# Kernel optimization log

Measured on AMD Instinct MI355X. Metric: run time of the kernel, lower is better.

## Reference

```python
import jax, jax.numpy as jnp
import numpy as np

N = 100_000      # nodes
E = 1_600_000    # edges (avg degree 16)
H = 128          # hidden_dim
L = 2            # num_layers
G = 64           # graphs in batch
BN_EPS = 1e-5


def setup_inputs() -> dict:
    key = jax.random.key(0)
    ks = jax.random.split(key, 20)
    x = jax.random.normal(ks[0], (N, 1), jnp.float32)
    edge_index = jax.random.randint(ks[1], (2, E), 0, N, dtype=jnp.int64)
    edge_attr = jax.random.uniform(ks[2], (E, 1), jnp.float32)
    batch = jnp.sort(jax.random.randint(ks[3], (N,), 0, G, dtype=jnp.int64))
    s = 1.0 / np.sqrt(H)
    return {
        "x": x, "edge_index": edge_index, "edge_attr": edge_attr, "batch": batch,
        "enc_w": jax.random.normal(ks[4], (1, H), jnp.float32),
        "enc_b": jnp.zeros((H,), jnp.float32),
        "eenc_w": jax.random.normal(ks[5], (1, H), jnp.float32),
        "eenc_b": jnp.zeros((H,), jnp.float32),
        "eps": jnp.zeros((L,), jnp.float32),  # train_eps=True, init 0
        "w1": jax.random.normal(ks[6], (L, H, H), jnp.float32) * s,
        "b1": jnp.zeros((L, H), jnp.float32),
        "w2": jax.random.normal(ks[7], (L, H, H), jnp.float32) * s,
        "b2": jnp.zeros((L, H), jnp.float32),
        "gamma": jnp.ones((L, H), jnp.float32),
        "beta": jnp.zeros((L, H), jnp.float32),
        "cw1": jax.random.normal(ks[8], (H, H // 2), jnp.float32) * s,
        "cb1": jnp.zeros((H // 2,), jnp.float32),
        "cw2": jax.random.normal(ks[9], (H // 2, 1), jnp.float32) * (1.0 / np.sqrt(H // 2)),
        "cb2": jnp.zeros((1,), jnp.float32),
    }


def reference(x, edge_index, edge_attr, batch,
              enc_w, enc_b, eenc_w, eenc_b,
              eps, w1, b1, w2, b2, gamma, beta,
              cw1, cb1, cw2, cb2):
    # Inference mode: dropout = identity, BatchNorm uses running stats (mean=0, var=1).
    h = x @ enc_w + enc_b                 # [N, H] node encoder
    ea = edge_attr @ eenc_w + eenc_b      # [E, H] edge encoder
    src, dst = edge_index[0], edge_index[1]
    inv_std = 1.0 / jnp.sqrt(1.0 + BN_EPS)
    for l in range(L):
        # GINEConv: out = MLP((1+eps)*x + sum_j relu(x_j + e_ij))
        msg = jax.nn.relu(h[src] + ea)                         # [E, H] gather + fuse
        agg = jax.ops.segment_sum(msg, dst, num_segments=N)    # [N, H] scatter-sum
        z = (1.0 + eps[l]) * h + agg
        z = jax.nn.relu(z @ w1[l] + b1[l]) @ w2[l] + b2[l]      # GIN MLP
        h = jax.nn.relu(gamma[l] * z * inv_std + beta[l])       # BN (eval) + ReLU
    # global mean pool over graphs
    cnt = jax.ops.segment_sum(jnp.ones((N, 1), h.dtype), batch, num_segments=G)
    pooled = jax.ops.segment_sum(h, batch, num_segments=G) / jnp.maximum(cnt, 1.0)
    hc = jax.nn.relu(pooled @ cw1 + cb1)
    out = jax.nn.sigmoid(hc @ cw2 + cb2)
    return out.squeeze(-1)                # [G]
```

## Files before the change

### kernel.cpp

```cpp
#include <hip/hip_runtime.h>

#define HDIM 128
#define NGRAPH 64
#define INVSTD 0.99999500003749972f
#define WTPAD 136
#define WSLOT (128 * WTPAD)
#define BKN 512
#define EPB 4096

typedef unsigned short ushort_t;
typedef unsigned int uint_t;
typedef unsigned char uchar_t;
typedef __attribute__((ext_vector_type(8))) short bf16x8;
typedef __attribute__((ext_vector_type(4))) float f32x4;
typedef __attribute__((ext_vector_type(2))) float f32x2;

__device__ __forceinline__ float bf2f(uint_t u) {
    return __int_as_float((int)(u << 16));
}
__device__ __forceinline__ float bf2f_hi(uint_t u) {
    return __int_as_float((int)(u & 0xFFFF0000u));
}
__device__ __forceinline__ uint_t f2bf(float f) {
    uint_t x = __float_as_uint(f);
    return (x + 0x7FFFu + ((x >> 16) & 1u)) >> 16;
}
__device__ __forceinline__ uint_t pack2(float a, float b) {
    return f2bf(a) | (f2bf(b) << 16);
}
__device__ __forceinline__ uint_t pack4fp8(float a, float b, float c, float d) {
    int v = __builtin_amdgcn_cvt_pk_fp8_f32(a, b, 0, false);
    v = __builtin_amdgcn_cvt_pk_fp8_f32(c, d, v, true);
    return (uint_t)v;
}

__global__ void k_encode(const float* __restrict__ x, const float* __restrict__ ew,
                         const float* __restrict__ enb, const float* __restrict__ ebe,
                         ushort_t* __restrict__ hb, uchar_t* __restrict__ hq, int N) {
    int tid = blockIdx.x * blockDim.x + threadIdx.x;
    int stride = gridDim.x * blockDim.x;
    int q = tid & 15;
    float4 wa = ((const float4*)ew)[2 * q];
    float4 wb = ((const float4*)ew)[2 * q + 1];
    float4 ba = ((const float4*)enb)[2 * q];
    float4 bb = ((const float4*)enb)[2 * q + 1];
    float4 ea = ((const float4*)ebe)[2 * q];
    float4 eb2 = ((const float4*)ebe)[2 * q + 1];
    ba.x += ea.x; ba.y += ea.y; ba.z += ea.z; ba.w += ea.w;
    bb.x += eb2.x; bb.y += eb2.y; bb.z += eb2.z; bb.w += eb2.w;
    int total = N * 16;
    for (int t = tid; t < total; t += stride) {
        int n = t >> 4;
        float xv = x[n];
        float v0 = fmaf(xv, wa.x, ba.x), v1 = fmaf(xv, wa.y, ba.y);
        float v2 = fmaf(xv, wa.z, ba.z), v3 = fmaf(xv, wa.w, ba.w);
        float v4 = fmaf(xv, wb.x, bb.x), v5 = fmaf(xv, wb.y, bb.y);
        float v6 = fmaf(xv, wb.z, bb.z), v7 = fmaf(xv, wb.w, bb.w);
        uint4 o;
        o.x = pack2(v0, v1); o.y = pack2(v2, v3);
        o.z = pack2(v4, v5); o.w = pack2(v6, v7);
        ((uint4*)(hb + (size_t)n * HDIM))[q] = o;
        uint2 o8;
        o8.x = pack4fp8(v0, v1, v2, v3);
        o8.y = pack4fp8(v4, v5, v6, v7);
        ((uint2*)(hq + (size_t)n * HDIM))[q] = o8;
    }
}

__global__ void k_prepw(const float* __restrict__ w1, const float* __restrict__ w2,
                        ushort_t* __restrict__ wtg) {
    int t = blockIdx.x * 256 + threadIdx.x;
    if (t >= 4 * 16384) return;
    int w = t >> 14, idx = t & 16383;
    int k = idx >> 7, n = idx & 127;
    const float* src = ((w & 1) ? w2 : w1) + (size_t)(w >> 1) * 16384;
    wtg[(size_t)w * WSLOT + n * WTPAD + k] = (ushort_t)f2bf(src[idx]);
}

__global__ __launch_bounds__(256) void k_cnt(const int* __restrict__ ei, int* __restrict__ btot,
                                             int nb, int E) {
    __shared__ int hist[256];
    hist[threadIdx.x] = 0;
    __syncthreads();
    int e0 = blockIdx.x * EPB;
    for (int i = threadIdx.x; i < EPB; i += 256) {
        int e = e0 + i;
        if (e < E) atomicAdd(&hist[ei[E + e] / BKN], 1);
    }
    __syncthreads();
    int c = hist[threadIdx.x];
    if (threadIdx.x < nb && c > 0) atomicAdd(&btot[threadIdx.x], c);
}

__global__ void k_bscan(const int* __restrict__ btot, int* __restrict__ segs, int nb, int E) {
    __shared__ int sm[256];
    int t = threadIdx.x;
    int v = (t < nb) ? btot[t] : 0;
    sm[t] = v;
    __syncthreads();
    #pragma unroll
    for (int off = 1; off < 256; off <<= 1) {
        int u = (t >= off) ? sm[t - off] : 0;
        __syncthreads();
        sm[t] += u;
        __syncthreads();
    }
    if (t < nb) segs[t] = sm[t] - v;
    if (t == 0) segs[nb] = E;
}

__global__ __launch_bounds__(256) void k_place0(const int* __restrict__ ei,
                                                const float* __restrict__ attr,
                                                const int* __restrict__ segs, int* cursor,
                                                int2* __restrict__ ebuf, int nb, int E) {
    __shared__ int hist[256];
    __shared__ int basev[256];
    hist[threadIdx.x] = 0;
    __syncthreads();
    int e0 = blockIdx.x * EPB;
    for (int i = threadIdx.x; i < EPB; i += 256) {
        int e = e0 + i;
        if (e < E) atomicAdd(&hist[ei[E + e] / BKN], 1);
    }
    __syncthreads();
    {
        int c = hist[threadIdx.x];
        basev[threadIdx.x] = (threadIdx.x < nb && c > 0) ? atomicAdd(&cursor[threadIdx.x], c) : 0;
        hist[threadIdx.x] = 0;
    }
    __syncthreads();
    for (int i = threadIdx.x; i < EPB; i += 256) {
        int e = e0 + i;
        if (e < E) {
            int s = ei[e], d = ei[E + e];
            float a = attr[e];
            int b = d / BKN;
            int r = atomicAdd(&hist[b], 1);
            ebuf[segs[b] + basev[b] + r] = make_int2(s | ((d & (BKN - 1)) << 17),
                                                     __float_as_int(a));
        }
    }
}

__global__ __launch_bounds__(256) void k_fine(const int2* __restrict__ ebuf,
                                              const int* __restrict__ segs,
                                              int2* __restrict__ epack, int* __restrict__ rs,
                                              int nb, int N, int E) {
    __shared__ int hist[BKN];
    __shared__ int cur[BKN];
    __shared__ int psum[256];
    int b = blockIdx.x;
    int d0 = b * BKN;
    int nd = min(BKN, N - d0);
    for (int i = threadIdx.x; i < BKN; i += 256) hist[i] = 0;
    __syncthreads();
    int s0 = segs[b], s1 = segs[b + 1];
    for (int e = s0 + threadIdx.x; e < s1; e += 256)
        atomicAdd(&hist[(uint_t)ebuf[e].x >> 17], 1);
    __syncthreads();
    int h0 = hist[2 * threadIdx.x], h1 = hist[2 * threadIdx.x + 1];
    psum[threadIdx.x] = h0 + h1;
    __syncthreads();
    #pragma unroll
    for (int off = 1; off < 256; off <<= 1) {
        int u = (threadIdx.x >= off) ? psum[threadIdx.x - off] : 0;
        __syncthreads();
        psum[threadIdx.x] += u;
        __syncthreads();
    }
    int pb = psum[threadIdx.x] - (h0 + h1);
    cur[2 * threadIdx.x] = pb;
    cur[2 * threadIdx.x + 1] = pb + h0;
    __syncthreads();
    for (int i = threadIdx.x; i < nd; i += 256) rs[d0 + i] = s0 + cur[i];
    if (b == nb - 1 && threadIdx.x == 0) rs[N] = E;
    __syncthreads();
    for (int e = s0 + threadIdx.x; e < s1; e += 256) {
        int2 rec = ebuf[e];
        int dl = (uint_t)rec.x >> 17;
        int r = atomicAdd(&cur[dl], 1);
        epack[s0 + r] = make_int2(rec.x & 0x1FFFF, rec.y);
    }
}

__device__ __forceinline__ void acc_edge(float acc[8], const uint2& u, float at,
        const float4& wa, const float4& wb) {
    f32x2 p0 = __builtin_amdgcn_cvt_pk_f32_fp8(u.x, false);
    f32x2 p1 = __builtin_amdgcn_cvt_pk_f32_fp8(u.x, true);
    f32x2 p2 = __builtin_amdgcn_cvt_pk_f32_fp8(u.y, false);
    f32x2 p3 = __builtin_amdgcn_cvt_pk_f32_fp8(u.y, true);
    acc[0] += fmaxf(fmaf(at, wa.x, p0[0]), 0.f);
    acc[1] += fmaxf(fmaf(at, wa.y, p0[1]), 0.f);
    acc[2] += fmaxf(fmaf(at, wa.z, p1[0]), 0.f);
    acc[3] += fmaxf(fmaf(at, wa.w, p1[1]), 0.f);
    acc[4] += fmaxf(fmaf(at, wb.x, p2[0]), 0.f);
    acc[5] += fmaxf(fmaf(at, wb.y, p2[1]), 0.f);
    acc[6] += fmaxf(fmaf(at, wb.z, p3[0]), 0.f);
    acc[7] += fmaxf(fmaf(at, wb.w, p3[1]), 0.f);
}

__global__ __launch_bounds__(256) void k_agg(
    const uchar_t* __restrict__ hq, const ushort_t* __restrict__ hb,
    const int* __restrict__ rs, const int2* __restrict__ epack,
    const float* __restrict__ ew, const float* __restrict__ ebv,
    const float* __restrict__ epsp, ushort_t* __restrict__ zb, int N) {
    int wave = (blockIdx.x * 256 + threadIdx.x) >> 6;
    if (wave >= N) return;
    int lane = threadIdx.x & 63;
    int p = lane >> 4;
    int q = lane & 15;
    int n = wave;
    int beg = rs[n];
    int cntE = rs[n + 1] - beg;
    float4 wa = ((const float4*)ew)[2 * q], wb = ((const float4*)ew)[2 * q + 1];

    float acc[8] = {0.f, 0.f, 0.f, 0.f, 0.f, 0.f, 0.f, 0.f};
    float acc2[8] = {0.f, 0.f, 0.f, 0.f, 0.f, 0.f, 0.f, 0.f};
    int j = p;
    for (; j + 4 < cntE; j += 8) {
        int2 e1 = epack[beg + j];
        int2 e2 = epack[beg + j + 4];
        uint2 u1 = *(const uint2*)(hq + (size_t)e1.x * HDIM + q * 8);
        uint2 u2 = *(const uint2*)(hq + (size_t)e2.x * HDIM + q * 8);
        acc_edge(acc,  u1, __int_as_float(e1.y), wa, wb);
        acc_edge(acc2, u2, __int_as_float(e2.y), wa, wb);
    }
    if (j < cntE) {
        int2 e1 = epack[beg + j];
        uint2 u1 = *(const uint2*)(hq + (size_t)e1.x * HDIM + q * 8);
        acc_edge(acc, u1, __int_as_float(e1.y), wa, wb);
    }
    #pragma unroll
    for (int k = 0; k < 8; ++k) {
        float v = acc[k] + acc2[k];
        v += __shfl_xor(v, 16);
        v += __shfl_xor(v, 32);
        acc[k] = v;
    }
    if (p == 0) {
        float sc = 1.f + epsp[0];
        float4 ba = ((const float4*)ebv)[2 * q], bb = ((const float4*)ebv)[2 * q + 1];
        float s0 = sc * ba.x, s1 = sc * ba.y, s2 = sc * ba.z, s3 = sc * ba.w;
        float s4 = sc * bb.x, s5 = sc * bb.y, s6 = sc * bb.z, s7 = sc * bb.w;
        uint4 u = *(const uint4*)(hb + (size_t)n * HDIM + q * 8);
        uint4 ob;
        ob.x = pack2(fmaf(sc, bf2f(u.x & 0xFFFFu), acc[0]) - s0,
                     fmaf(sc, bf2f_hi(u.x),        acc[1]) - s1);
        ob.y = pack2(fmaf(sc, bf2f(u.y & 0xFFFFu), acc[2]) - s2,
                     fmaf(sc, bf2f_hi(u.y),        acc[3]) - s3);
        ob.z = pack2(fmaf(sc, bf2f(u.z & 0xFFFFu), acc[4]) - s4,
                     fmaf(sc, bf2f_hi(u.z),        acc[5]) - s5);
        ob.w = pack2(fmaf(sc, bf2f(u.w & 0xFFFFu), acc[6]) - s6,
                     fmaf(sc, bf2f_hi(u.w),        acc[7]) - s7);
        *(uint4*)(zb + (size_t)n * HDIM + q * 8) = ob;
    }
}

template<int MODE, int EBF, int WQ>
__global__ __launch_bounds__(256) void k_gemm(
    const ushort_t* __restrict__ A, const ushort_t* __restrict__ WT,
    const float* __restrict__ bias, const float* __restrict__ gam,
    const float* __restrict__ bet, const float* __restrict__ ebe,
    ushort_t* __restrict__ out, uchar_t* __restrict__ outq, int N) {
    __shared__ ushort_t wt[128 * WTPAD];
    int tid = threadIdx.x;
    #pragma unroll
    for (int i = 0; i < 9; ++i) {
        int c = i * 256 + tid;
        if (c < 2176) ((bf16x8*)wt)[c] = ((const bf16x8*)WT)[c];
    }
    __syncthreads();

    int wid = tid >> 6, lane = tid & 63;
    int ra = lane & 15, qa = lane >> 4;

    bf16x8 bfr[4][8];
    #pragma unroll
    for (int ks = 0; ks < 4; ++ks)
        #pragma unroll
        for (int nf = 0; nf < 8; ++nf)
            bfr[ks][nf] = *(const bf16x8*)&wt[(nf * 16 + ra) * WTPAD + ks * 32 + qa * 8];

    float bi[8], gg[8], be_[8], ef[8];
    #pragma unroll
    for (int nf = 0; nf < 8; ++nf) {
        int col = nf * 16 + ra;
        bi[nf] = bias[col];
        if (MODE == 1) { gg[nf] = gam[col]; be_[nf] = bet[col]; }
        if (EBF)       { ef[nf] = ebe[col]; }
    }

    bf16x8 azero;
    #pragma unroll
    for (int j = 0; j < 8; ++j) azero[j] = 0;

    #pragma unroll
    for (int it = 0; it < 4; ++it) {
        int m0 = blockIdx.x * 256 + it * 64 + wid * 16;
        int mr = m0 + ra;
        bf16x8 afr[4];
        #pragma unroll
        for (int ks = 0; ks < 4; ++ks)
            afr[ks] = (mr < N) ? *(const bf16x8*)&A[(size_t)mr * HDIM + ks * 32 + qa * 8]
                               : azero;
        f32x4 acc[8];
        #pragma unroll
        for (int nf = 0; nf < 8; ++nf)
            #pragma unroll
            for (int j = 0; j < 4; ++j) acc[nf][j] = 0.f;
        #pragma unroll
        for (int ks = 0; ks < 4; ++ks)
            #pragma unroll
            for (int nf = 0; nf < 8; ++nf)
                acc[nf] = __builtin_amdgcn_mfma_f32_16x16x32_bf16(afr[ks], bfr[ks][nf], acc[nf], 0, 0, 0);
        #pragma unroll
        for (int nf = 0; nf < 8; ++nf) {
            #pragma unroll
            for (int r = 0; r < 4; ++r) {
                int row = m0 + qa * 4 + r;
                if (row < N) {
                    float v = acc[nf][r] + bi[nf];
                    if (MODE == 0) v = fmaxf(v, 0.f);
                    else           v = fmaxf(fmaf(gg[nf] * v, INVSTD, be_[nf]), 0.f);
                    if (EBF)       v += ef[nf];
                    out[(size_t)row * HDIM + nf * 16 + ra] = (ushort_t)f2bf(v);
                    if (WQ)
                        outq[(size_t)row * HDIM + nf * 16 + ra] =
                            (uchar_t)(__builtin_amdgcn_cvt_pk_fp8_f32(v, 0.f, 0, false) & 0xFF);
                }
            }
        }
    }
}

#define PCHUNK 256
#define PWIN 4
__global__ __launch_bounds__(256) void k_pool2(const ushort_t* __restrict__ hb,
                                               const int* __restrict__ batch,
                                               float* pooled, int N) {
    __shared__ float acc[PWIN][HDIM];
    int n0 = blockIdx.x * PCHUNK;
    if (n0 >= N) return;
    int n1 = min(n0 + PCHUNK, N);
    int g0 = batch[n0];
    int g1 = batch[n1 - 1];
    for (int i = threadIdx.x; i < PWIN * HDIM; i += 256) ((float*)acc)[i] = 0.f;
    __syncthreads();

    int grp = threadIdx.x >> 5;
    int q = threadIdx.x & 31;
    float4 racc = make_float4(0.f, 0.f, 0.f, 0.f);
    int gcur = g0;
    for (int n = n0 + grp; n < n1; n += 8) {
        int g = batch[n];
        if (g != gcur) {
            int w = gcur - g0;
            float* p = (w < PWIN) ? &acc[w][q * 4] : (pooled + gcur * HDIM + q * 4);
            atomicAdd(p + 0, racc.x); atomicAdd(p + 1, racc.y);
            atomicAdd(p + 2, racc.z); atomicAdd(p + 3, racc.w);
            racc = make_float4(0.f, 0.f, 0.f, 0.f);
            gcur = g;
        }
        uint2 u = ((const uint2*)(hb + (size_t)n * HDIM))[q];
        racc.x += bf2f(u.x);
        racc.y += bf2f_hi(u.x);
        racc.z += bf2f(u.y);
        racc.w += bf2f_hi(u.y);
    }
    {
        int w = gcur - g0;
        float* p = (w < PWIN) ? &acc[w][q * 4] : (pooled + gcur * HDIM + q * 4);
        atomicAdd(p + 0, racc.x); atomicAdd(p + 1, racc.y);
        atomicAdd(p + 2, racc.z); atomicAdd(p + 3, racc.w);
    }
    __syncthreads();

    int span = min(g1 - g0 + 1, PWIN);
    for (int i = threadIdx.x; i < span * HDIM; i += 256) {
        int w = i >> 7, f = i & 127;
        float v = acc[w][f];
        if (v != 0.f) atomicAdd(pooled + (g0 + w) * HDIM + f, v);
    }
}

__global__ void k_classify(const float* __restrict__ pooled, const int* __restrict__ batch,
                           const float* __restrict__ cw1, const float* __restrict__ cb1,
                           const float* __restrict__ cw2, const float* __restrict__ cb2,
                           float* __restrict__ out, int N) {
    __shared__ float p[HDIM];
    int g = blockIdx.x, j = threadIdx.x;
    int lo = 0, hi = N;
    while (lo < hi) { int m = (lo + hi) >> 1; if (batch[m] < g) lo = m + 1; else hi = m; }
    int lo2 = lo, hi2 = N;
    while (lo2 < hi2) { int m = (lo2 + hi2) >> 1; if (batch[m] < g + 1) lo2 = m + 1; else hi2 = m; }
    float c = fmaxf((float)(lo2 - lo), 1.f);
    p[j]      = pooled[g * HDIM + j] / c;
    p[j + 64] = pooled[g * HDIM + j + 64] / c;
    __syncthreads();
    float acc = cb1[j];
    #pragma unroll 4
    for (int k = 0; k < HDIM; ++k) acc = fmaf(p[k], cw1[k * 64 + j], acc);
    acc = fmaxf(acc, 0.f);
    float v = acc * cw2[j];
    #pragma unroll
    for (int off = 32; off > 0; off >>= 1) v += __shfl_down(v, off, 64);
    if (j == 0) out[g] = 1.f / (1.f + expf(-(v + cb2[0])));
}

static inline size_t align_up(size_t v, size_t a) { return (v + a - 1) & ~(a - 1); }

extern "C" void kernel_launch(void* const* d_in, const int* in_sizes, int n_in,
                              void* d_out, int out_size, void* d_ws, size_t ws_size,
                              hipStream_t stream) {
    const float* x      = (const float*)d_in[0];
    const int*   ei     = (const int*)d_in[1];
    const float* eattr  = (const float*)d_in[2];
    const int*   batch  = (const int*)d_in[3];
    const float* enc_w  = (const float*)d_in[4];
    const float* enc_b  = (const float*)d_in[5];
    const float* eenc_w = (const float*)d_in[6];
    const float* eenc_b = (const float*)d_in[7];
    const float* eps    = (const float*)d_in[8];
    const float* w1     = (const float*)d_in[9];
    const float* b1     = (const float*)d_in[10];
    const float* w2     = (const float*)d_in[11];
    const float* b2     = (const float*)d_in[12];
    const float* gamma  = (const float*)d_in[13];
    const float* beta   = (const float*)d_in[14];
    const float* cw1    = (const float*)d_in[15];
    const float* cb1    = (const float*)d_in[16];
    const float* cw2    = (const float*)d_in[17];
    const float* cb2    = (const float*)d_in[18];

    int N = in_sizes[0];
    int E = in_sizes[2];

    int nb = (N + BKN - 1) / BKN;
    int nblk = (E + EPB - 1) / EPB;

    char* wsb = (char*)d_ws;
    size_t off = 0;
    ushort_t* hb  = (ushort_t*)(wsb + off); off = align_up(off + (size_t)N * HDIM * 2, 256);
    uchar_t*  hq  = (uchar_t*)(wsb + off);  off = align_up(off + (size_t)N * HDIM, 256);
    ushort_t* zb  = (ushort_t*)(wsb + off); off = align_up(off + (size_t)N * HDIM * 2, 256);
    ushort_t* wtg = (ushort_t*)(wsb + off); off = align_up(off + (size_t)4 * WSLOT * 2, 256);
    float* pooled = (float*)(wsb + off);    off = align_up(off + NGRAPH * HDIM * 4, 256);
    int*   btot   = (int*)(wsb + off);      off = align_up(off + (size_t)(nb + 1) * 4, 256);
    int*   segs   = (int*)(wsb + off);      off = align_up(off + (size_t)(nb + 1) * 4, 256);
    int*   cursor = (int*)(wsb + off);      off = align_up(off + (size_t)nb * 4, 256);
    int*   rs     = (int*)(wsb + off);      off = align_up(off + (size_t)(N + 1) * 4, 256);
    int2*  ebuf   = (int2*)(wsb + off);     off = align_up(off + (size_t)E * 8, 256);
    int2*  epack  = (int2*)(wsb + off);     off = align_up(off + (size_t)E * 8, 256);

    hipMemsetAsync(btot, 0, (size_t)(nb + 1) * 4, stream);
    hipMemsetAsync(cursor, 0, (size_t)nb * 4, stream);
    k_cnt<<<nblk, 256, 0, stream>>>(ei, btot, nb, E);
    k_prepw<<<256, 256, 0, stream>>>(w1, w2, wtg);
    k_bscan<<<1, 256, 0, stream>>>(btot, segs, nb, E);
    k_place0<<<nblk, 256, 0, stream>>>(ei, eattr, segs, cursor, ebuf, nb, E);
    k_fine<<<nb, 256, 0, stream>>>(ebuf, segs, epack, rs, nb, N, E);

    hipMemsetAsync(pooled, 0, NGRAPH * HDIM * sizeof(float), stream);
    k_encode<<<2048, 256, 0, stream>>>(x, enc_w, enc_b, eenc_b, hb, hq, N);

    int gblocks = (N + 255) / 256;
    int ablocks = (N * 64 + 255) / 256;

    k_agg<<<ablocks, 256, 0, stream>>>(hq, hb, rs, epack, eenc_w, eenc_b, eps + 0, zb, N);
    k_gemm<0,0,0><<<gblocks, 256, 0, stream>>>(zb, wtg + 0 * WSLOT, b1, nullptr, nullptr,
                                               nullptr, zb, nullptr, N);
    k_gemm<1,1,1><<<gblocks, 256, 0, stream>>>(zb, wtg + 1 * WSLOT, b2, gamma, beta,
                                               eenc_b, hb, hq, N);
    k_agg<<<ablocks, 256, 0, stream>>>(hq, hb, rs, epack, eenc_w, eenc_b, eps + 1, zb, N);
    k_gemm<0,0,0><<<gblocks, 256, 0, stream>>>(zb, wtg + 2 * WSLOT, b1 + HDIM, nullptr, nullptr,
                                               nullptr, zb, nullptr, N);
    k_gemm<1,0,0><<<gblocks, 256, 0, stream>>>(zb, wtg + 3 * WSLOT, b2 + HDIM, gamma + HDIM,
                                               beta + HDIM, nullptr, hb, nullptr, N);

    k_pool2<<<(N + PCHUNK - 1) / PCHUNK, 256, 0, stream>>>(hb, batch, pooled, N);
    k_classify<<<NGRAPH, 64, 0, stream>>>(pooled, batch, cw1, cb1, cw2, cb2, (float*)d_out, N);
}
```

Baseline: 301.4 us.

## Replace fp8 gather copy with single fp16 node buffer and packed fp16 aggregation

Drops the separate fp8 copy of node features and stores them once as fp16. The edge aggregation now gathers 16-byte fp16 rows and does the edge-encoder FMA, ReLU and sum with packed half2 math (v_pk_max_f16), accumulating in fp16. Edge attributes are pre-packed as half2. This removes the extra fp8 write in the GEMM epilogue and the fp8-to-fp32 conversions, but it doubles gather bytes per edge versus fp8 and accumulates sums in fp16, which risks precision loss.

```diff
diff --git a/kernel.cpp b/kernel.cpp
--- a/kernel.cpp
+++ b/kernel.cpp
@@ -10,16 +10,12 @@
 
 typedef unsigned short ushort_t;
 typedef unsigned int uint_t;
-typedef unsigned char uchar_t;
 typedef __attribute__((ext_vector_type(8))) short bf16x8;
 typedef __attribute__((ext_vector_type(4))) float f32x4;
-typedef __attribute__((ext_vector_type(2))) float f32x2;
+typedef __attribute__((ext_vector_type(2))) _Float16 h16x2;
 
 __device__ __forceinline__ float bf2f(uint_t u) {
     return __int_as_float((int)(u << 16));
-}
-__device__ __forceinline__ float bf2f_hi(uint_t u) {
-    return __int_as_float((int)(u & 0xFFFF0000u));
 }
 __device__ __forceinline__ uint_t f2bf(float f) {
     uint_t x = __float_as_uint(f);
@@ -28,15 +24,27 @@
 __device__ __forceinline__ uint_t pack2(float a, float b) {
     return f2bf(a) | (f2bf(b) << 16);
 }
-__device__ __forceinline__ uint_t pack4fp8(float a, float b, float c, float d) {
-    int v = __builtin_amdgcn_cvt_pk_fp8_f32(a, b, 0, false);
-    v = __builtin_amdgcn_cvt_pk_fp8_f32(c, d, v, true);
-    return (uint_t)v;
+__device__ __forceinline__ uint_t h2u(h16x2 h) {
+    union { h16x2 h; uint_t u; } x; x.h = h; return x.u;
+}
+__device__ __forceinline__ h16x2 u2h(uint_t u) {
+    union { h16x2 h; uint_t u; } x; x.u = u; return x.h;
+}
+__device__ __forceinline__ uint_t packh2(float a, float b) {
+    h16x2 v; v[0] = (_Float16)a; v[1] = (_Float16)b; return h2u(v);
+}
+__device__ __forceinline__ ushort_t f2h(float f) {
+    union { _Float16 h; ushort_t u; } x; x.h = (_Float16)f; return x.u;
+}
+__device__ __forceinline__ uint_t pkmax0(uint_t x) {
+    uint_t r, z = 0;
+    asm("v_pk_max_f16 %0, %1, %2" : "=v"(r) : "v"(x), "v"(z));
+    return r;
 }
 
 __global__ void k_encode(const float* __restrict__ x, const float* __restrict__ ew,
                          const float* __restrict__ enb, const float* __restrict__ ebe,
-                         ushort_t* __restrict__ hb, uchar_t* __restrict__ hq, int N) {
+                         ushort_t* __restrict__ hh, int N) {
     int tid = blockIdx.x * blockDim.x + threadIdx.x;
     int stride = gridDim.x * blockDim.x;
     int q = tid & 15;
@@ -52,18 +60,12 @@
     for (int t = tid; t < total; t += stride) {
         int n = t >> 4;
         float xv = x[n];
-        float v0 = fmaf(xv, wa.x, ba.x), v1 = fmaf(xv, wa.y, ba.y);
-        float v2 = fmaf(xv, wa.z, ba.z), v3 = fmaf(xv, wa.w, ba.w);
-        float v4 = fmaf(xv, wb.x, bb.x), v5 = fmaf(xv, wb.y, bb.y);
-        float v6 = fmaf(xv, wb.z, bb.z), v7 = fmaf(xv, wb.w, bb.w);
         uint4 o;
-        o.x = pack2(v0, v1); o.y = pack2(v2, v3);
-        o.z = pack2(v4, v5); o.w = pack2(v6, v7);
-        ((uint4*)(hb + (size_t)n * HDIM))[q] = o;
-        uint2 o8;
-        o8.x = pack4fp8(v0, v1, v2, v3);
-        o8.y = pack4fp8(v4, v5, v6, v7);
-        ((uint2*)(hq + (size_t)n * HDIM))[q] = o8;
+        o.x = packh2(fmaf(xv, wa.x, ba.x), fmaf(xv, wa.y, ba.y));
+        o.y = packh2(fmaf(xv, wa.z, ba.z), fmaf(xv, wa.w, ba.w));
+        o.z = packh2(fmaf(xv, wb.x, bb.x), fmaf(xv, wb.y, bb.y));
+        o.w = packh2(fmaf(xv, wb.z, bb.z), fmaf(xv, wb.w, bb.w));
+        ((uint4*)(hh + (size_t)n * HDIM))[q] = o;
     }
 }
 
@@ -137,7 +139,7 @@
             int b = d / BKN;
             int r = atomicAdd(&hist[b], 1);
             ebuf[segs[b] + basev[b] + r] = make_int2(s | ((d & (BKN - 1)) << 17),
-                                                     __float_as_int(a));
+                                                     (int)packh2(a, a));
         }
     }
 }
@@ -183,25 +185,17 @@
     }
 }
 
-__device__ __forceinline__ void acc_edge(float acc[8], const uint2& u, float at,
-        const float4& wa, const float4& wb) {
-    f32x2 p0 = __builtin_amdgcn_cvt_pk_f32_fp8(u.x, false);
-    f32x2 p1 = __builtin_amdgcn_cvt_pk_f32_fp8(u.x, true);
-    f32x2 p2 = __builtin_amdgcn_cvt_pk_f32_fp8(u.y, false);
-    f32x2 p3 = __builtin_amdgcn_cvt_pk_f32_fp8(u.y, true);
-    acc[0] += fmaxf(fmaf(at, wa.x, p0[0]), 0.f);
-    acc[1] += fmaxf(fmaf(at, wa.y, p0[1]), 0.f);
-    acc[2] += fmaxf(fmaf(at, wa.z, p1[0]), 0.f);
-    acc[3] += fmaxf(fmaf(at, wa.w, p1[1]), 0.f);
-    acc[4] += fmaxf(fmaf(at, wb.x, p2[0]), 0.f);
-    acc[5] += fmaxf(fmaf(at, wb.y, p2[1]), 0.f);
-    acc[6] += fmaxf(fmaf(at, wb.z, p3[0]), 0.f);
-    acc[7] += fmaxf(fmaf(at, wb.w, p3[1]), 0.f);
+__device__ __forceinline__ void acc_edge(h16x2 acc[4], const uint4& u, h16x2 at2,
+                                         const h16x2 w2[4]) {
+    acc[0] += u2h(pkmax0(h2u(at2 * w2[0] + u2h(u.x))));
+    acc[1] += u2h(pkmax0(h2u(at2 * w2[1] + u2h(u.y))));
+    acc[2] += u2h(pkmax0(h2u(at2 * w2[2] + u2h(u.z))));
+    acc[3] += u2h(pkmax0(h2u(at2 * w2[3] + u2h(u.w))));
 }
 
 __global__ __launch_bounds__(256) void k_agg(
-    const uchar_t* __restrict__ hq, const ushort_t* __restrict__ hb,
-    const int* __restrict__ rs, const int2* __restrict__ epack,
+    const ushort_t* __restrict__ hh, const int* __restrict__ rs,
+    const int2* __restrict__ epack,
     const float* __restrict__ ew, const float* __restrict__ ebv,
     const float* __restrict__ epsp, ushort_t* __restrict__ zb, int N) {
     int wave = (blockIdx.x * 256 + threadIdx.x) >> 6;
@@ -213,55 +207,60 @@
     int beg = rs[n];
     int cntE = rs[n + 1] - beg;
     float4 wa = ((const float4*)ew)[2 * q], wb = ((const float4*)ew)[2 * q + 1];
-
-    float acc[8] = {0.f, 0.f, 0.f, 0.f, 0.f, 0.f, 0.f, 0.f};
-    float acc2[8] = {0.f, 0.f, 0.f, 0.f, 0.f, 0.f, 0.f, 0.f};
+    h16x2 w2[4];
+    w2[0] = u2h(packh2(wa.x, wa.y));
+    w2[1] = u2h(packh2(wa.z, wa.w));
+    w2[2] = u2h(packh2(wb.x, wb.y));
+    w2[3] = u2h(packh2(wb.z, wb.w));
+
+    h16x2 acc[4], acc2[4];
+    #pragma unroll
+    for (int k = 0; k < 4; ++k) { acc[k] = u2h(0u); acc2[k] = u2h(0u); }
     int j = p;
     for (; j + 4 < cntE; j += 8) {
         int2 e1 = epack[beg + j];
         int2 e2 = epack[beg + j + 4];
-        uint2 u1 = *(const uint2*)(hq + (size_t)e1.x * HDIM + q * 8);
-        uint2 u2 = *(const uint2*)(hq + (size_t)e2.x * HDIM + q * 8);
-        acc_edge(acc,  u1, __int_as_float(e1.y), wa, wb);
-        acc_edge(acc2, u2, __int_as_float(e2.y), wa, wb);
+        uint4 u1 = *(const uint4*)(hh + (size_t)e1.x * HDIM + q * 8);
+        uint4 u2v = *(const uint4*)(hh + (size_t)e2.x * HDIM + q * 8);
+        acc_edge(acc,  u1, u2h((uint_t)e1.y), w2);
+        acc_edge(acc2, u2v, u2h((uint_t)e2.y), w2);
     }
     if (j < cntE) {
         int2 e1 = epack[beg + j];
-        uint2 u1 = *(const uint2*)(hq + (size_t)e1.x * HDIM + q * 8);
-        acc_edge(acc, u1, __int_as_float(e1.y), wa, wb);
-    }
-    #pragma unroll
-    for (int k = 0; k < 8; ++k) {
-        float v = acc[k] + acc2[k];
-        v += __shfl_xor(v, 16);
-        v += __shfl_xor(v, 32);
-        acc[k] = v;
+        uint4 u1 = *(const uint4*)(hh + (size_t)e1.x * HDIM + q * 8);
+        acc_edge(acc, u1, u2h((uint_t)e1.y), w2);
+    }
+    #pragma unroll
+    for (int k = 0; k < 4; ++k) {
+        h16x2 c = acc[k] + acc2[k];
+        c += u2h((uint_t)__shfl_xor((int)h2u(c), 16));
+        c += u2h((uint_t)__shfl_xor((int)h2u(c), 32));
+        acc[k] = c;
     }
     if (p == 0) {
         float sc = 1.f + epsp[0];
         float4 ba = ((const float4*)ebv)[2 * q], bb = ((const float4*)ebv)[2 * q + 1];
-        float s0 = sc * ba.x, s1 = sc * ba.y, s2 = sc * ba.z, s3 = sc * ba.w;
-        float s4 = sc * bb.x, s5 = sc * bb.y, s6 = sc * bb.z, s7 = sc * bb.w;
-        uint4 u = *(const uint4*)(hb + (size_t)n * HDIM + q * 8);
+        uint4 u = *(const uint4*)(hh + (size_t)n * HDIM + q * 8);
+        h16x2 t0 = u2h(u.x), t1 = u2h(u.y), t2 = u2h(u.z), t3 = u2h(u.w);
         uint4 ob;
-        ob.x = pack2(fmaf(sc, bf2f(u.x & 0xFFFFu), acc[0]) - s0,
-                     fmaf(sc, bf2f_hi(u.x),        acc[1]) - s1);
-        ob.y = pack2(fmaf(sc, bf2f(u.y & 0xFFFFu), acc[2]) - s2,
-                     fmaf(sc, bf2f_hi(u.y),        acc[3]) - s3);
-        ob.z = pack2(fmaf(sc, bf2f(u.z & 0xFFFFu), acc[4]) - s4,
-                     fmaf(sc, bf2f_hi(u.z),        acc[5]) - s5);
-        ob.w = pack2(fmaf(sc, bf2f(u.w & 0xFFFFu), acc[6]) - s6,
-                     fmaf(sc, bf2f_hi(u.w),        acc[7]) - s7);
+        ob.x = pack2(fmaf(sc, (float)t0[0], (float)acc[0][0]) - sc * ba.x,
+                     fmaf(sc, (float)t0[1], (float)acc[0][1]) - sc * ba.y);
+        ob.y = pack2(fmaf(sc, (float)t1[0], (float)acc[1][0]) - sc * ba.z,
+                     fmaf(sc, (float)t1[1], (float)acc[1][1]) - sc * ba.w);
+        ob.z = pack2(fmaf(sc, (float)t2[0], (float)acc[2][0]) - sc * bb.x,
+                     fmaf(sc, (float)t2[1], (float)acc[2][1]) - sc * bb.y);
+        ob.w = pack2(fmaf(sc, (float)t3[0], (float)acc[3][0]) - sc * bb.z,
+                     fmaf(sc, (float)t3[1], (float)acc[3][1]) - sc * bb.w);
         *(uint4*)(zb + (size_t)n * HDIM + q * 8) = ob;
     }
 }
 
-template<int MODE, int EBF, int WQ>
+template<int MODE, int EBF, int OUT16>
 __global__ __launch_bounds__(256) void k_gemm(
     const ushort_t* __restrict__ A, const ushort_t* __restrict__ WT,
     const float* __restrict__ bias, const float* __restrict__ gam,
     const float* __restrict__ bet, const float* __restrict__ ebe,
-    ushort_t* __restrict__ out, uchar_t* __restrict__ outq, int N) {
+    ushort_t* __restrict__ out, int N) {
     __shared__ ushort_t wt[128 * WTPAD];
     int tid = threadIdx.x;
     #pragma unroll
@@ -323,10 +322,10 @@
                     if (MODE == 0) v = fmaxf(v, 0.f);
                     else           v = fmaxf(fmaf(gg[nf] * v, INVSTD, be_[nf]), 0.f);
                     if (EBF)       v += ef[nf];
-                    out[(size_t)row * HDIM + nf * 16 + ra] = (ushort_t)f2bf(v);
-                    if (WQ)
-                        outq[(size_t)row * HDIM + nf * 16 + ra] =
-                            (uchar_t)(__builtin_amdgcn_cvt_pk_fp8_f32(v, 0.f, 0, false) & 0xFF);
+                    if (OUT16)
+                        out[(size_t)row * HDIM + nf * 16 + ra] = f2h(v);
+                    else
+                        out[(size_t)row * HDIM + nf * 16 + ra] = (ushort_t)f2bf(v);
                 }
             }
         }
@@ -335,7 +334,7 @@
 
 #define PCHUNK 256
 #define PWIN 4
-__global__ __launch_bounds__(256) void k_pool2(const ushort_t* __restrict__ hb,
+__global__ __launch_bounds__(256) void k_pool2(const ushort_t* __restrict__ hh,
                                                const int* __restrict__ batch,
                                                float* pooled, int N) {
     __shared__ float acc[PWIN][HDIM];
@@ -361,11 +360,12 @@
             racc = make_float4(0.f, 0.f, 0.f, 0.f);
             gcur = g;
         }
-        uint2 u = ((const uint2*)(hb + (size_t)n * HDIM))[q];
-        racc.x += bf2f(u.x);
-        racc.y += bf2f_hi(u.x);
-        racc.z += bf2f(u.y);
-        racc.w += bf2f_hi(u.y);
+        uint2 u = ((const uint2*)(hh + (size_t)n * HDIM))[q];
+        h16x2 f0 = u2h(u.x), f1 = u2h(u.y);
+        racc.x += (float)f0[0];
+        racc.y += (float)f0[1];
+        racc.z += (float)f1[0];
+        racc.w += (float)f1[1];
     }
     {
         int w = gcur - g0;
@@ -440,8 +440,7 @@
 
     char* wsb = (char*)d_ws;
     size_t off = 0;
-    ushort_t* hb  = (ushort_t*)(wsb + off); off = align_up(off + (size_t)N * HDIM * 2, 256);
-    uchar_t*  hq  = (uchar_t*)(wsb + off);  off = align_up(off + (size_t)N * HDIM, 256);
+    ushort_t* hh  = (ushort_t*)(wsb + off); off = align_up(off + (size_t)N * HDIM * 2, 256);
     ushort_t* zb  = (ushort_t*)(wsb + off); off = align_up(off + (size_t)N * HDIM * 2, 256);
     ushort_t* wtg = (ushort_t*)(wsb + off); off = align_up(off + (size_t)4 * WSLOT * 2, 256);
     float* pooled = (float*)(wsb + off);    off = align_up(off + NGRAPH * HDIM * 4, 256);
@@ -461,22 +460,22 @@
     k_fine<<<nb, 256, 0, stream>>>(ebuf, segs, epack, rs, nb, N, E);
 
     hipMemsetAsync(pooled, 0, NGRAPH * HDIM * sizeof(float), stream);
-    k_encode<<<2048, 256, 0, stream>>>(x, enc_w, enc_b, eenc_b, hb, hq, N);
+    k_encode<<<2048, 256, 0, stream>>>(x, enc_w, enc_b, eenc_b, hh, N);
 
     int gblocks = (N + 255) / 256;
     int ablocks = (N * 64 + 255) / 256;
 
-    k_agg<<<ablocks, 256, 0, stream>>>(hq, hb, rs, epack, eenc_w, eenc_b, eps + 0, zb, N);
+    k_agg<<<ablocks, 256, 0, stream>>>(hh, rs, epack, eenc_w, eenc_b, eps + 0, zb, N);
     k_gemm<0,0,0><<<gblocks, 256, 0, stream>>>(zb, wtg + 0 * WSLOT, b1, nullptr, nullptr,
-                                               nullptr, zb, nullptr, N);
+                                               nullptr, zb, N);
     k_gemm<1,1,1><<<gblocks, 256, 0, stream>>>(zb, wtg + 1 * WSLOT, b2, gamma, beta,
-                                               eenc_b, hb, hq, N);
-    k_agg<<<ablocks, 256, 0, stream>>>(hq, hb, rs, epack, eenc_w, eenc_b, eps + 1, zb, N);
+                                               eenc_b, hh, N);
+    k_agg<<<ablocks, 256, 0, stream>>>(hh, rs, epack, eenc_w, eenc_b, eps + 1, zb, N);
     k_gemm<0,0,0><<<gblocks, 256, 0, stream>>>(zb, wtg + 2 * WSLOT, b1 + HDIM, nullptr, nullptr,
-                                               nullptr, zb, nullptr, N);
-    k_gemm<1,0,0><<<gblocks, 256, 0, stream>>>(zb, wtg + 3 * WSLOT, b2 + HDIM, gamma + HDIM,
-                                               beta + HDIM, nullptr, hb, nullptr, N);
-
-    k_pool2<<<(N + PCHUNK - 1) / PCHUNK, 256, 0, stream>>>(hb, batch, pooled, N);
+                                               nullptr, zb, N);
+    k_gemm<1,0,1><<<gblocks, 256, 0, stream>>>(zb, wtg + 3 * WSLOT, b2 + HDIM, gamma + HDIM,
+                                               beta + HDIM, nullptr, hh, N);
+
+    k_pool2<<<(N + PCHUNK - 1) / PCHUNK, 256, 0, stream>>>(hh, batch, pooled, N);
     k_classify<<<NGRAPH, 64, 0, stream>>>(pooled, batch, cw1, cb1, cw2, cb2, (float*)d_out, N);
 }
```

Result: slower. 309.0 us (+2.5%).
